# Kernel optimization log

Measured on AMD Instinct MI355X. Metric: run time of the kernel, lower is better.

Reference implementation:

```python
import jax, jax.numpy as jnp
import numpy as np

B, T, C = 4, 2048, 1024
H, HS = 16, 64  # n_heads, head_size; H*HS == C


def setup_inputs() -> dict:
    key = jax.random.key(0)
    ks = jax.random.split(key, 6)
    s = 0.02
    x = jax.random.normal(ks[0], (B, T, C), dtype=jnp.float32)
    Wq = jax.random.normal(ks[1], (H, C, HS), dtype=jnp.float32) * s
    Wk = jax.random.normal(ks[2], (H, C, HS), dtype=jnp.float32) * s
    Wv = jax.random.normal(ks[3], (H, C, HS), dtype=jnp.float32) * s
    Wo = jax.random.normal(ks[4], (C, C), dtype=jnp.float32) * s
    bo = jnp.zeros((C,), dtype=jnp.float32)
    return {"x": x, "Wq": Wq, "Wk": Wk, "Wv": Wv, "Wo": Wo, "bo": bo}


def reference(x, Wq, Wk, Wv, Wo, bo):
    # batched multi-head causal attention (math identical to per-head loop)
    q = jnp.einsum('btc,hcd->bhtd', x, Wq)  # [B,H,T,HS]
    k = jnp.einsum('btc,hcd->bhtd', x, Wk)
    v = jnp.einsum('btc,hcd->bhtd', x, Wv)
    scale = 1.0 / jnp.sqrt(jnp.asarray(HS, x.dtype))
    scores = jnp.einsum('bhtd,bhsd->bhts', q, k) * scale  # [B,H,T,T]
    causal = jnp.tril(jnp.ones((T, T), dtype=bool))
    scores = jnp.where(causal, scores, jnp.asarray(-jnp.inf, scores.dtype))
    attn = jax.nn.softmax(scores, axis=-1)
    out = jnp.einsum('bhts,bhsd->bhtd', attn, v)  # [B,H,T,HS]
    # concat heads along feature dim (head order == module list order)
    out = out.transpose(0, 2, 1, 3).reshape(B, T, C)
    return out @ Wo.T + bo
```

## Files before the change

### kernel.cpp

```cpp
#include <hip/hip_runtime.h>

typedef __attribute__((ext_vector_type(8))) short v8s;
typedef __attribute__((ext_vector_type(4))) short v4s;
typedef __attribute__((ext_vector_type(4))) float v4f;

static __device__ __forceinline__ short f2bf(float f) {
  union { float f; unsigned u; } c; c.f = f;
  unsigned r = c.u + 0x7fffu + ((c.u >> 16) & 1u);
  return (short)(r >> 16);
}

static __device__ __forceinline__ unsigned pk_bf16(float a, float b) {
  union { float f; unsigned u; } ca, cb; ca.f = a; cb.f = b;
  return ((ca.u + 0x8000u) >> 16) | ((cb.u + 0x8000u) & 0xffff0000u);
}

#if __has_builtin(__builtin_amdgcn_exp2f)
#define EXP2(x) __builtin_amdgcn_exp2f(x)
#else
#define EXP2(x) exp2f(x)
#endif

#define GLDS(gp, lp) __builtin_amdgcn_global_load_lds( \
    (const __attribute__((address_space(1))) void*)(gp), \
    (__attribute__((address_space(3))) void*)(lp), 16, 0, 0)


__global__ __launch_bounds__(256) void prep(const float* __restrict__ x,
                                            const float* __restrict__ Wq,
                                            const float* __restrict__ Wk,
                                            const float* __restrict__ Wv,
                                            const float* __restrict__ Wo,
                                            short* __restrict__ Xb,
                                            short* __restrict__ Wot,
                                            short* __restrict__ Wt) {
  __shared__ float tile[64][65];
  const int blk = blockIdx.x;
  const int tid = threadIdx.x;
  if (blk < 9216) {
    const float* src = (blk < 8192) ? x : Wo;
    short* dst = (blk < 8192) ? Xb : Wot;
    const int b2 = (blk < 8192) ? blk : (blk - 8192);
    const int idx = (b2 * 256 + tid) * 4;
    float4 v = *(const float4*)(src + idx);
    v4s o; o.x = f2bf(v.x); o.y = f2bf(v.y); o.z = f2bf(v.z); o.w = f2bf(v.w);
    *(v4s*)(dst + idx) = o;
    return;
  }
  const int bb = blk - 9216;
  const int sel = bb >> 8, rest = bb & 255;
  const int h = rest >> 4, kt = rest & 15;
  const float* W = (sel == 0) ? Wq : ((sel == 1) ? Wk : Wv);
  const int k0 = kt * 64;
  for (int i = 0; i < 4; ++i) {
    int c = i * 256 + tid;
    int row = c >> 4, c4 = (c & 15) * 4;
    float4 v = *(const float4*)(W + (size_t)h * 65536 + (size_t)(k0 + row) * 64 + c4);
    tile[row][c4 + 0] = v.x; tile[row][c4 + 1] = v.y;
    tile[row][c4 + 2] = v.z; tile[row][c4 + 3] = v.w;
  }
  __syncthreads();
  for (int i = 0; i < 2; ++i) {
    int c = i * 256 + tid;
    int d = c >> 3, k8 = (c & 7) * 8;
    v8s o;
    for (int j = 0; j < 8; ++j) o[j] = f2bf(tile[k8 + j][d]);
    *(v8s*)(Wt + (size_t)(sel * 1024 + h * 64 + d) * 1024 + k0 + k8) = o;
  }
}


__global__ __launch_bounds__(512) void gemm_qkv(const short* __restrict__ Xb,
                                                const short* __restrict__ Wt,
                                                short* __restrict__ Qo,
                                                short* __restrict__ Ko,
                                                short* __restrict__ Vt) {
  __shared__ short lds[49152];
  const int tid = threadIdx.x;
  const int lane = tid & 63, quad = lane >> 4, l16 = lane & 15;
  const int wave = tid >> 6;
  const int m0 = blockIdx.x * 256, n0 = blockIdx.y * 128;
  const int wm = (wave >> 1) * 64, wn = (wave & 1) * 64;

  const int r0 = tid >> 2, cbs = (tid & 3) ^ ((r0 >> 1) & 3);
  const size_t offA0 = (size_t)(m0 + r0) * 1024 + cbs * 8;
  const size_t offB0 = (size_t)(n0 + r0) * 1024 + cbs * 8;

  int aoff[4], boff[4];
#pragma unroll
  for (int mt = 0; mt < 4; ++mt) {
    int row = wm + mt * 16 + l16;
    aoff[mt] = row * 32 + (quad ^ ((row >> 1) & 3)) * 8;
  }
#pragma unroll
  for (int nt = 0; nt < 4; ++nt) {
    int row = wn + nt * 16 + l16;
    boff[nt] = row * 32 + (quad ^ ((row >> 1) & 3)) * 8;
  }

  v4f acc[4][4];
#pragma unroll
  for (int i = 0; i < 4; ++i)
#pragma unroll
    for (int j = 0; j < 4; ++j) acc[i][j] = (v4f){0.f, 0.f, 0.f, 0.f};

#pragma unroll
  for (int t = 0; t < 3; ++t) {
    GLDS(Xb + offA0 + t * 32, lds + t * 8192 + tid * 8);
    GLDS(Xb + offA0 + 131072 + t * 32, lds + t * 8192 + 4096 + tid * 8);
    GLDS(Wt + offB0 + t * 32, lds + 32768 + t * 4096 + tid * 8);
  }
  asm volatile("s_waitcnt vmcnt(6)" ::: "memory");
  __builtin_amdgcn_s_barrier();

#pragma unroll 4
  for (int t = 0; t < 32; ++t) {
    const int p = t & 3;
    int tn = t + 3; if (tn > 31) tn = 31;
    const int pn = (t + 3) & 3;
    const short* lAp = lds + p * 8192;
    const short* lBp = lds + 32768 + p * 4096;

    GLDS(Xb + offA0 + tn * 32, lds + pn * 8192 + tid * 8);
    GLDS(Xb + offA0 + 131072 + tn * 32, lds + pn * 8192 + 4096 + tid * 8);
    v8s a[4], b[2];
#pragma unroll
    for (int mt = 0; mt < 4; ++mt) a[mt] = *(const v8s*)(lAp + aoff[mt]);
    b[0] = *(const v8s*)(lBp + boff[0]);
    b[1] = *(const v8s*)(lBp + boff[1]);
    __builtin_amdgcn_s_setprio(1);
#pragma unroll
    for (int mt = 0; mt < 4; ++mt) {
      acc[mt][0] = __builtin_amdgcn_mfma_f32_16x16x32_bf16(a[mt], b[0], acc[mt][0], 0, 0, 0);
      acc[mt][1] = __builtin_amdgcn_mfma_f32_16x16x32_bf16(a[mt], b[1], acc[mt][1], 0, 0, 0);
    }
    __builtin_amdgcn_s_setprio(0);

    GLDS(Wt + offB0 + tn * 32, lds + 32768 + pn * 4096 + tid * 8);
    b[0] = *(const v8s*)(lBp + boff[2]);
    b[1] = *(const v8s*)(lBp + boff[3]);
    __builtin_amdgcn_s_setprio(1);
#pragma unroll
    for (int mt = 0; mt < 4; ++mt) {
      acc[mt][2] = __builtin_amdgcn_mfma_f32_16x16x32_bf16(a[mt], b[0], acc[mt][2], 0, 0, 0);
      acc[mt][3] = __builtin_amdgcn_mfma_f32_16x16x32_bf16(a[mt], b[1], acc[mt][3], 0, 0, 0);
    }
    __builtin_amdgcn_s_setprio(0);

    asm volatile("s_waitcnt vmcnt(6) lgkmcnt(0)" ::: "memory");
    __builtin_amdgcn_s_barrier();
  }

  const int selu = n0 >> 10;
  if (selu < 2) {
    short* obase = (selu == 0) ? Qo : Ko;
#pragma unroll
    for (int nt = 0; nt < 4; ++nt) {
      int n = (n0 + wn + nt * 16 + l16) & 1023;
      int h = n >> 6, d = n & 63;
#pragma unroll
      for (int mt = 0; mt < 4; ++mt) {
        int m = m0 + wm + mt * 16 + quad * 4;
        int b_ = m >> 11, tt_ = m & 2047;
        size_t base = (size_t)((b_ * 16 + h) * 2048 + tt_) * 64 + d;
#pragma unroll
        for (int r = 0; r < 4; ++r)
          obase[base + (size_t)r * 64] = f2bf(acc[mt][nt][r]);
      }
    }
  } else {
#pragma unroll
    for (int nt = 0; nt < 4; ++nt) {
      int n = (n0 + wn + nt * 16 + l16) & 1023;
      int h = n >> 6, d = n & 63;
#pragma unroll
      for (int mt = 0; mt < 4; ++mt) {
        int m = m0 + wm + mt * 16 + quad * 4;
        int b_ = m >> 11, tt_ = m & 2047;
        int2 dw;
        dw.x = (int)pk_bf16(acc[mt][nt][0], acc[mt][nt][1]);
        dw.y = (int)pk_bf16(acc[mt][nt][2], acc[mt][nt][3]);
        *(int2*)(Vt + ((size_t)(b_ * 16 + h) * 64 + d) * 2048 + tt_) = dw;
      }
    }
  }
}


#define ASTAGE(P, KB)                                                             \
  GLDS(K + qkbase + (size_t)((KB) + r0) * 64 + cl0 * 8, lK + (P) * 4096 + tid * 8);          \
  GLDS(K + qkbase + (size_t)((KB) + r1) * 64 + cl1 * 8, lK + (P) * 4096 + tid * 8 + 2048);   \
  GLDS(Vt + vtbase + (size_t)r0 * 2048 + (KB) + cl0 * 8, lV + (P) * 4096 + tid * 8);         \
  GLDS(Vt + vtbase + (size_t)r1 * 2048 + (KB) + cl1 * 8, lV + (P) * 4096 + tid * 8 + 2048)

__global__ __launch_bounds__(256, 2) void attn(const short* __restrict__ Q,
                                               const short* __restrict__ K,
                                               const short* __restrict__ Vt,
                                               short* __restrict__ AO) {
  __shared__ short lK[2 * 64 * 64];
  __shared__ short lV[2 * 64 * 64];
  __shared__ short lP[4 * 16 * 64];
  const int tid = threadIdx.x;
  const int w = tid >> 6, lane = tid & 63, quad = lane >> 4, l16 = lane & 15;
  const int bh = blockIdx.x & 63;
  const int slot = blockIdx.x >> 6;
  const int c = (int)((0x5410672398DCABEFull >> (slot * 4)) & 15ull);
  const float kexp = 0.18033688011112042f;
  const unsigned psel = 0x07060302u;
  short* pw = lP + w * 1024;
  const size_t qkbase = (size_t)bh * 2048 * 64;
  const size_t vtbase = (size_t)bh * 64 * 2048;
  const int b_ = bh >> 4, h = bh & 15;

  const int r0 = tid >> 3, cp = tid & 7;
  const int cl0 = cp ^ (r0 & 7);
  const int r1 = r0 + 32;
  const int cl1 = cp ^ (r1 & 7);

  const int swz = l16 & 7;
  const int ph0 = (quad ^ swz) * 8;
  const int ph1 = ((quad + 4) ^ swz) * 8;

  const int qc = c * 128 + w * 32;

  v8s bQ[2][2];
#pragma unroll
  for (int qs = 0; qs < 2; ++qs) {
    const short* qb = Q + qkbase + (size_t)(qc + qs * 16 + l16) * 64 + quad * 8;
    bQ[qs][0] = *(const v8s*)(qb);
    bQ[qs][1] = *(const v8s*)(qb + 32);
  }
  v4f accO[2][4];
#pragma unroll
  for (int qs = 0; qs < 2; ++qs)
#pragma unroll
    for (int g = 0; g < 4; ++g) accO[qs][g] = (v4f){0.f, 0.f, 0.f, 0.f};
  float lrun[2] = {0.f, 0.f};

  const int nst = 2 * c + 2;

  ASTAGE(0, 0);

  for (int kt = 0; kt < nst; ++kt) {
    const int p = kt & 1;
    const int kb = kt * 64;
    if (kt + 1 < nst) {
      ASTAGE(p ^ 1, kb + 64);
      asm volatile("s_waitcnt vmcnt(4)" ::: "memory");
    } else {
      asm volatile("s_waitcnt vmcnt(0)" ::: "memory");
    }
    __builtin_amdgcn_s_barrier();
    const short* lKp = lK + p * 4096;
    const short* lVp = lV + p * 4096;

    const bool act0 = kb < qc + 16;
    const bool act1 = kb < qc + 32;
    if (act1) {
      v4f sT[2][4];
      {
        v8s aK[4][2];
#pragma unroll
        for (int mt = 0; mt < 4; ++mt) {
          const short* kr = lKp + (mt * 16 + l16) * 64;
          aK[mt][0] = *(const v8s*)(kr + ph0);
          aK[mt][1] = *(const v8s*)(kr + ph1);
        }
        __builtin_amdgcn_s_setprio(1);
#pragma unroll
        for (int qs = 0; qs < 2; ++qs) {
          if (qs == 0 ? !act0 : false) continue;
#pragma unroll
          for (int mt = 0; mt < 4; ++mt) {
            v4f t = (v4f){0.f, 0.f, 0.f, 0.f};
            t = __builtin_amdgcn_mfma_f32_16x16x32_bf16(aK[mt][0], bQ[qs][0], t, 0, 0, 0);
            t = __builtin_amdgcn_mfma_f32_16x16x32_bf16(aK[mt][1], bQ[qs][1], t, 0, 0, 0);
            sT[qs][mt] = t;
          }
        }
        __builtin_amdgcn_s_setprio(0);
      }
      v8s aV[4][2];
#pragma unroll
      for (int g = 0; g < 4; ++g) {
        const short* vr = lVp + (g * 16 + l16) * 64;
        aV[g][0] = *(const v8s*)(vr + ph0);
        aV[g][1] = *(const v8s*)(vr + ph1);
      }
#pragma unroll
      for (int qs = 0; qs < 2; ++qs) {
        if (qs == 0 ? !act0 : false) continue;
        const int rbase = qc + qs * 16;
        if (kb + 63 >= rbase) {
          const int kq = kb + quad * 4 - (rbase + l16);
#pragma unroll
          for (int mt = 0; mt < 4; ++mt)
#pragma unroll
            for (int r = 0; r < 4; ++r)
              if (kq + mt * 16 + r > 0) sT[qs][mt][r] = -__builtin_inff();
        }
        float ls = lrun[qs];
#pragma unroll
        for (int mt = 0; mt < 4; ++mt) {
          float p0 = EXP2(sT[qs][mt][0] * kexp);
          float p1 = EXP2(sT[qs][mt][1] * kexp);
          float p2 = EXP2(sT[qs][mt][2] * kexp);
          float p3 = EXP2(sT[qs][mt][3] * kexp);
          ls += (p0 + p1) + (p2 + p3);
          int2 dw;
          dw.x = (int)__builtin_amdgcn_perm(__float_as_uint(p1), __float_as_uint(p0), psel);
          dw.y = (int)__builtin_amdgcn_perm(__float_as_uint(p3), __float_as_uint(p2), psel);
          *(int2*)&pw[l16 * 64 + ((mt * 16 + quad * 4) ^ (swz * 8))] = dw;
        }
        lrun[qs] = ls;
        v8s bP0 = *(const v8s*)&pw[l16 * 64 + ph0];
        v8s bP1 = *(const v8s*)&pw[l16 * 64 + ph1];
        __builtin_amdgcn_s_setprio(1);
#pragma unroll
        for (int g = 0; g < 4; ++g) {
          accO[qs][g] = __builtin_amdgcn_mfma_f32_16x16x32_bf16(aV[g][0], bP0, accO[qs][g], 0, 0, 0);
          accO[qs][g] = __builtin_amdgcn_mfma_f32_16x16x32_bf16(aV[g][1], bP1, accO[qs][g], 0, 0, 0);
        }
        __builtin_amdgcn_s_setprio(0);
      }
    }
    __builtin_amdgcn_s_barrier();
  }

#pragma unroll
  for (int qs = 0; qs < 2; ++qs) {
    float ls = lrun[qs];
    ls += __shfl_xor(ls, 16);
    ls += __shfl_xor(ls, 32);
    float inv = __builtin_amdgcn_rcpf(ls);
    int t = qc + qs * 16 + l16;
    short* ao = AO + ((size_t)(b_ * 2048 + t)) * 1024 + h * 64 + quad * 4;
#pragma unroll
    for (int g = 0; g < 4; ++g) {
      int2 dw;
      dw.x = (int)pk_bf16(accO[qs][g][0] * inv, accO[qs][g][1] * inv);
      dw.y = (int)pk_bf16(accO[qs][g][2] * inv, accO[qs][g][3] * inv);
      *(int2*)(ao + g * 16) = dw;
    }
  }
}

#undef ASTAGE


__global__ __launch_bounds__(512) void gemm_out(const short* __restrict__ AO,
                                                const short* __restrict__ Wot,
                                                const float* __restrict__ bo,
                                                float* __restrict__ out) {
  __shared__ short lds[49152];
  const int tid = threadIdx.x;
  const int lane = tid & 63, quad = lane >> 4, l16 = lane & 15;
  const int wave = tid >> 6;
  const int m0 = blockIdx.x * 256, n0 = blockIdx.y * 128;
  const int wm = (wave >> 1) * 64, wn = (wave & 1) * 64;

  const int r0 = tid >> 2, cbs = (tid & 3) ^ ((r0 >> 1) & 3);
  const size_t offA0 = (size_t)(m0 + r0) * 1024 + cbs * 8;
  const size_t offB0 = (size_t)(n0 + r0) * 1024 + cbs * 8;

  int aoff[4], boff[4];
#pragma unroll
  for (int mt = 0; mt < 4; ++mt) {
    int row = wm + mt * 16 + l16;
    aoff[mt] = row * 32 + (quad ^ ((row >> 1) & 3)) * 8;
  }
#pragma unroll
  for (int nt = 0; nt < 4; ++nt) {
    int row = wn + nt * 16 + l16;
    boff[nt] = row * 32 + (quad ^ ((row >> 1) & 3)) * 8;
  }

  v4f acc[4][4];
#pragma unroll
  for (int i = 0; i < 4; ++i)
#pragma unroll
    for (int j = 0; j < 4; ++j) acc[i][j] = (v4f){0.f, 0.f, 0.f, 0.f};

#pragma unroll
  for (int t = 0; t < 3; ++t) {
    GLDS(AO + offA0 + t * 32, lds + t * 8192 + tid * 8);
    GLDS(AO + offA0 + 131072 + t * 32, lds + t * 8192 + 4096 + tid * 8);
    GLDS(Wot + offB0 + t * 32, lds + 32768 + t * 4096 + tid * 8);
  }
  asm volatile("s_waitcnt vmcnt(6)" ::: "memory");
  __builtin_amdgcn_s_barrier();

#pragma unroll 4
  for (int t = 0; t < 32; ++t) {
    const int p = t & 3;
    int tn = t + 3; if (tn > 31) tn = 31;
    const int pn = (t + 3) & 3;
    const short* lAp = lds + p * 8192;
    const short* lBp = lds + 32768 + p * 4096;

    GLDS(AO + offA0 + tn * 32, lds + pn * 8192 + tid * 8);
    GLDS(AO + offA0 + 131072 + tn * 32, lds + pn * 8192 + 4096 + tid * 8);
    v8s a[4], b[2];
#pragma unroll
    for (int mt = 0; mt < 4; ++mt) a[mt] = *(const v8s*)(lAp + aoff[mt]);
    b[0] = *(const v8s*)(lBp + boff[0]);
    b[1] = *(const v8s*)(lBp + boff[1]);
    __builtin_amdgcn_s_setprio(1);
#pragma unroll
    for (int mt = 0; mt < 4; ++mt) {
      acc[mt][0] = __builtin_amdgcn_mfma_f32_16x16x32_bf16(a[mt], b[0], acc[mt][0], 0, 0, 0);
      acc[mt][1] = __builtin_amdgcn_mfma_f32_16x16x32_bf16(a[mt], b[1], acc[mt][1], 0, 0, 0);
    }
    __builtin_amdgcn_s_setprio(0);

    GLDS(Wot + offB0 + tn * 32, lds + 32768 + pn * 4096 + tid * 8);
    b[0] = *(const v8s*)(lBp + boff[2]);
    b[1] = *(const v8s*)(lBp + boff[3]);
    __builtin_amdgcn_s_setprio(1);
#pragma unroll
    for (int mt = 0; mt < 4; ++mt) {
      acc[mt][2] = __builtin_amdgcn_mfma_f32_16x16x32_bf16(a[mt], b[0], acc[mt][2], 0, 0, 0);
      acc[mt][3] = __builtin_amdgcn_mfma_f32_16x16x32_bf16(a[mt], b[1], acc[mt][3], 0, 0, 0);
    }
    __builtin_amdgcn_s_setprio(0);

    asm volatile("s_waitcnt vmcnt(6) lgkmcnt(0)" ::: "memory");
    __builtin_amdgcn_s_barrier();
  }

#pragma unroll
  for (int nt = 0; nt < 4; ++nt) {
    int n = n0 + wn + nt * 16 + l16;
    float bias = bo[n];
#pragma unroll
    for (int mt = 0; mt < 4; ++mt) {
      int m = m0 + wm + mt * 16 + quad * 4;
#pragma unroll
      for (int r = 0; r < 4; ++r)
        out[(size_t)(m + r) * 1024 + n] = acc[mt][nt][r] + bias;
    }
  }
}


extern "C" void kernel_launch(void* const* d_in, const int* in_sizes, int n_in,
                              void* d_out, int out_size, void* d_ws, size_t ws_size,
                              hipStream_t stream) {
  const float* x  = (const float*)d_in[0];
  const float* Wq = (const float*)d_in[1];
  const float* Wk = (const float*)d_in[2];
  const float* Wv = (const float*)d_in[3];
  const float* Wo = (const float*)d_in[4];
  const float* bo = (const float*)d_in[5];
  float* out = (float*)d_out;
  char* ws = (char*)d_ws;

  short* Xb  = (short*)(ws);
  short* Wt  = (short*)(ws + (16u << 20));
  short* Wot = (short*)(ws + (22u << 20));
  short* Q   = (short*)(ws + (24u << 20));
  short* K   = (short*)(ws + (40u << 20));
  short* Vt  = (short*)(ws + (56u << 20));

  prep<<<9984, 256, 0, stream>>>(x, Wq, Wk, Wv, Wo, Xb, Wot, Wt);
  gemm_qkv<<<dim3(32, 24), 512, 0, stream>>>(Xb, Wt, Q, K, Vt);
  attn<<<1024, 256, 0, stream>>>(Q, K, Vt, Xb);
  gemm_out<<<dim3(32, 8), 512, 0, stream>>>(Xb, Wot, bo, out);
}
```

Before: 226.1 us.

## Use BK=64 triple-buffered QKV GEMM and fold softmax scale into Q

The QKV projection GEMM moves from a 4-stage pipeline with 32-wide K tiles to a 3-stage pipeline with 64-wide K tiles and an XOR swizzle over 8 chunks, halving loop iterations and barriers and issuing 16 MFMAs per half-step. The softmax exponent scale (1/sqrt(d)·log2e) is now applied to Q when it is written out, removing a multiply per score element in the attention kernel. This costs more LDS (144KB per block), and rounding Q after scaling changes numerics slightly.

```diff
diff --git a/kernel.cpp b/kernel.cpp
--- a/kernel.cpp
+++ b/kernel.cpp
@@ -70,33 +70,39 @@
 }
 
 
+#define GQ_STAGE_A(P, T) do {                                                     \
+  _Pragma("unroll") for (int i_ = 0; i_ < 4; ++i_)                                \
+    GLDS(Xb + (size_t)(m0 + rA + i_ * 64) * 1024 + (T) * 64 + cbl * 8,            \
+         lds + (P) * 16384 + (tid + i_ * 512) * 8); } while (0)
+
+#define GQ_STAGE_B(P, T) do {                                                     \
+  _Pragma("unroll") for (int i_ = 0; i_ < 2; ++i_)                                \
+    GLDS(Wt + (size_t)(n0 + rA + i_ * 64) * 1024 + (T) * 64 + cbl * 8,            \
+         lds + 49152 + (P) * 8192 + (tid + i_ * 512) * 8); } while (0)
+
 __global__ __launch_bounds__(512) void gemm_qkv(const short* __restrict__ Xb,
                                                 const short* __restrict__ Wt,
                                                 short* __restrict__ Qo,
                                                 short* __restrict__ Ko,
                                                 short* __restrict__ Vt) {
-  __shared__ short lds[49152];
+  __shared__ short lds[73728];
   const int tid = threadIdx.x;
   const int lane = tid & 63, quad = lane >> 4, l16 = lane & 15;
   const int wave = tid >> 6;
   const int m0 = blockIdx.x * 256, n0 = blockIdx.y * 128;
   const int wm = (wave >> 1) * 64, wn = (wave & 1) * 64;
 
-  const int r0 = tid >> 2, cbs = (tid & 3) ^ ((r0 >> 1) & 3);
-  const size_t offA0 = (size_t)(m0 + r0) * 1024 + cbs * 8;
-  const size_t offB0 = (size_t)(n0 + r0) * 1024 + cbs * 8;
-
+  const int rA = tid >> 3;
+  const int cbl = (tid & 7) ^ (rA & 7);
+
+  const int swz = l16 & 7;
+  const int csw0 = (quad ^ swz) * 8;
+  const int csw1 = ((4 + quad) ^ swz) * 8;
   int aoff[4], boff[4];
 #pragma unroll
-  for (int mt = 0; mt < 4; ++mt) {
-    int row = wm + mt * 16 + l16;
-    aoff[mt] = row * 32 + (quad ^ ((row >> 1) & 3)) * 8;
-  }
-#pragma unroll
-  for (int nt = 0; nt < 4; ++nt) {
-    int row = wn + nt * 16 + l16;
-    boff[nt] = row * 32 + (quad ^ ((row >> 1) & 3)) * 8;
-  }
+  for (int mt = 0; mt < 4; ++mt) aoff[mt] = (wm + mt * 16 + l16) * 64;
+#pragma unroll
+  for (int nt = 0; nt < 4; ++nt) boff[nt] = (wn + nt * 16 + l16) * 64;
 
   v4f acc[4][4];
 #pragma unroll
@@ -104,56 +110,56 @@
 #pragma unroll
     for (int j = 0; j < 4; ++j) acc[i][j] = (v4f){0.f, 0.f, 0.f, 0.f};
 
-#pragma unroll
-  for (int t = 0; t < 3; ++t) {
-    GLDS(Xb + offA0 + t * 32, lds + t * 8192 + tid * 8);
-    GLDS(Xb + offA0 + 131072 + t * 32, lds + t * 8192 + 4096 + tid * 8);
-    GLDS(Wt + offB0 + t * 32, lds + 32768 + t * 4096 + tid * 8);
-  }
+  GQ_STAGE_A(0, 0); GQ_STAGE_B(0, 0);
+  GQ_STAGE_A(1, 1); GQ_STAGE_B(1, 1);
   asm volatile("s_waitcnt vmcnt(6)" ::: "memory");
   __builtin_amdgcn_s_barrier();
 
-#pragma unroll 4
-  for (int t = 0; t < 32; ++t) {
-    const int p = t & 3;
-    int tn = t + 3; if (tn > 31) tn = 31;
-    const int pn = (t + 3) & 3;
-    const short* lAp = lds + p * 8192;
-    const short* lBp = lds + 32768 + p * 4096;
-
-    GLDS(Xb + offA0 + tn * 32, lds + pn * 8192 + tid * 8);
-    GLDS(Xb + offA0 + 131072 + tn * 32, lds + pn * 8192 + 4096 + tid * 8);
-    v8s a[4], b[2];
-#pragma unroll
-    for (int mt = 0; mt < 4; ++mt) a[mt] = *(const v8s*)(lAp + aoff[mt]);
-    b[0] = *(const v8s*)(lBp + boff[0]);
-    b[1] = *(const v8s*)(lBp + boff[1]);
+  int p = 0, pn = 2;
+#pragma unroll 1
+  for (int t = 0; t < 16; ++t) {
+    int tn = t + 2; if (tn > 15) tn = 15;
+    const short* lAp = lds + p * 16384;
+    const short* lBp = lds + 49152 + p * 8192;
+
+    GQ_STAGE_A(pn, tn);
+    v8s a[4], b[4];
+#pragma unroll
+    for (int mt = 0; mt < 4; ++mt) a[mt] = *(const v8s*)(lAp + aoff[mt] + csw0);
+#pragma unroll
+    for (int nt = 0; nt < 4; ++nt) b[nt] = *(const v8s*)(lBp + boff[nt] + csw0);
     __builtin_amdgcn_s_setprio(1);
 #pragma unroll
-    for (int mt = 0; mt < 4; ++mt) {
-      acc[mt][0] = __builtin_amdgcn_mfma_f32_16x16x32_bf16(a[mt], b[0], acc[mt][0], 0, 0, 0);
-      acc[mt][1] = __builtin_amdgcn_mfma_f32_16x16x32_bf16(a[mt], b[1], acc[mt][1], 0, 0, 0);
-    }
+    for (int mt = 0; mt < 4; ++mt)
+#pragma unroll
+      for (int nt = 0; nt < 4; ++nt)
+        acc[mt][nt] = __builtin_amdgcn_mfma_f32_16x16x32_bf16(a[mt], b[nt], acc[mt][nt], 0, 0, 0);
     __builtin_amdgcn_s_setprio(0);
 
-    GLDS(Wt + offB0 + tn * 32, lds + 32768 + pn * 4096 + tid * 8);
-    b[0] = *(const v8s*)(lBp + boff[2]);
-    b[1] = *(const v8s*)(lBp + boff[3]);
+    GQ_STAGE_B(pn, tn);
+#pragma unroll
+    for (int mt = 0; mt < 4; ++mt) a[mt] = *(const v8s*)(lAp + aoff[mt] + csw1);
+#pragma unroll
+    for (int nt = 0; nt < 4; ++nt) b[nt] = *(const v8s*)(lBp + boff[nt] + csw1);
     __builtin_amdgcn_s_setprio(1);
 #pragma unroll
-    for (int mt = 0; mt < 4; ++mt) {
-      acc[mt][2] = __builtin_amdgcn_mfma_f32_16x16x32_bf16(a[mt], b[0], acc[mt][2], 0, 0, 0);
-      acc[mt][3] = __builtin_amdgcn_mfma_f32_16x16x32_bf16(a[mt], b[1], acc[mt][3], 0, 0, 0);
-    }
+    for (int mt = 0; mt < 4; ++mt)
+#pragma unroll
+      for (int nt = 0; nt < 4; ++nt)
+        acc[mt][nt] = __builtin_amdgcn_mfma_f32_16x16x32_bf16(a[mt], b[nt], acc[mt][nt], 0, 0, 0);
     __builtin_amdgcn_s_setprio(0);
 
     asm volatile("s_waitcnt vmcnt(6) lgkmcnt(0)" ::: "memory");
     __builtin_amdgcn_s_barrier();
-  }
+    p = (p == 2) ? 0 : p + 1;
+    pn = (pn == 2) ? 0 : pn + 1;
+  }
+  asm volatile("s_waitcnt vmcnt(0)" ::: "memory");
 
   const int selu = n0 >> 10;
   if (selu < 2) {
     short* obase = (selu == 0) ? Qo : Ko;
+    const float sc = (selu == 0) ? 0.18033688011112042f : 1.0f;
 #pragma unroll
     for (int nt = 0; nt < 4; ++nt) {
       int n = (n0 + wn + nt * 16 + l16) & 1023;
@@ -165,7 +171,7 @@
         size_t base = (size_t)((b_ * 16 + h) * 2048 + tt_) * 64 + d;
 #pragma unroll
         for (int r = 0; r < 4; ++r)
-          obase[base + (size_t)r * 64] = f2bf(acc[mt][nt][r]);
+          obase[base + (size_t)r * 64] = f2bf(acc[mt][nt][r] * sc);
       }
     }
   } else {
@@ -205,7 +211,6 @@
   const int bh = blockIdx.x & 63;
   const int slot = blockIdx.x >> 6;
   const int c = (int)((0x5410672398DCABEFull >> (slot * 4)) & 15ull);
-  const float kexp = 0.18033688011112042f;
   const unsigned psel = 0x07060302u;
   short* pw = lP + w * 1024;
   const size_t qkbase = (size_t)bh * 2048 * 64;
@@ -302,10 +307,10 @@
         float ls = lrun[qs];
 #pragma unroll
         for (int mt = 0; mt < 4; ++mt) {
-          float p0 = EXP2(sT[qs][mt][0] * kexp);
-          float p1 = EXP2(sT[qs][mt][1] * kexp);
-          float p2 = EXP2(sT[qs][mt][2] * kexp);
-          float p3 = EXP2(sT[qs][mt][3] * kexp);
+          float p0 = EXP2(sT[qs][mt][0]);
+          float p1 = EXP2(sT[qs][mt][1]);
+          float p2 = EXP2(sT[qs][mt][2]);
+          float p3 = EXP2(sT[qs][mt][3]);
           ls += (p0 + p1) + (p2 + p3);
           int2 dw;
           dw.x = (int)__builtin_amdgcn_perm(__float_as_uint(p1), __float_as_uint(p0), psel);
```

Result: slower. 236.0 us (+4.4%).
